# Kernel tuning notes

Hardware: AMD Instinct MI355X
Metric: run time of the kernel (lower is better)

## Reference

```python
import jax, jax.numpy as jnp
import numpy as np

N = 50000      # nodes
E = 800000     # directed edges
IN = 64        # in_dim
ED = 16        # edge_dim
H = 8          # heads
D = 32         # hdim (per-head out channels)
NM = 500       # molecules (graphs)
SLOPE = 0.2    # GATConv negative_slope
MLP_SLOPE = 0.01  # torch LeakyReLU default in the Sequential


def _glorot(k, shape, fan_in):
    return jax.random.normal(k, shape, jnp.float32) * (1.0 / np.sqrt(fan_in))


def setup_inputs() -> dict:
    key = jax.random.key(0)
    ks = jax.random.split(key, 32)
    inp = {}
    inp["x"] = jax.random.normal(ks[0], (N, IN), jnp.float32)
    inp["edge_index"] = jax.random.randint(ks[1], (2, E), 0, N)
    inp["edge_attr"] = jax.random.normal(ks[2], (E, ED), jnp.float32)
    inp["batch"] = jnp.sort(jax.random.randint(ks[3], (N,), 0, NM))
    ins = [IN, H * D, H * D]
    i = 4
    for l in range(3):
        inp[f"W{l+1}"] = _glorot(ks[i], (ins[l], H * D), ins[l]); i += 1
        inp[f"as{l+1}"] = _glorot(ks[i], (H, D), D); i += 1
        inp[f"ad{l+1}"] = _glorot(ks[i], (H, D), D); i += 1
        inp[f"We{l+1}"] = _glorot(ks[i], (ED, H * D), ED); i += 1
        inp[f"ae{l+1}"] = _glorot(ks[i], (H, D), D); i += 1
        inp[f"b{l+1}"] = jnp.zeros((H * D,), jnp.float32); i += 1
    # final MLP: 4*H*D -> 3*D -> 2*D -> 1
    inp["lw1"] = _glorot(ks[i], (4 * H * D, 3 * D), 4 * H * D); i += 1
    inp["lb1"] = jnp.zeros((3 * D,), jnp.float32)
    inp["lw2"] = _glorot(ks[i], (3 * D, 2 * D), 3 * D); i += 1
    inp["lb2"] = jnp.zeros((2 * D,), jnp.float32)
    inp["lw3"] = _glorot(ks[i], (2 * D, 1), 2 * D); i += 1
    inp["lb3"] = jnp.zeros((1,), jnp.float32)
    return inp


def _gat_conv(x, src, dst, ea, W, a_s, a_d, We, a_e, b):
    n = x.shape[0]
    xl = (x @ W).reshape(n, H, D)           # [N,H,D]
    el = (ea @ We).reshape(-1, H, D)        # [E',H,D]
    a_src = jnp.einsum('nhd,hd->nh', xl, a_s)
    a_dst = jnp.einsum('nhd,hd->nh', xl, a_d)
    a_edg = jnp.einsum('ehd,hd->eh', el, a_e)
    alpha = a_src[src] + a_dst[dst] + a_edg         # [E',H]
    alpha = jax.nn.leaky_relu(alpha, SLOPE)
    amax = jax.ops.segment_max(alpha, dst, num_segments=n)
    ex = jnp.exp(alpha - amax[dst])
    den = jax.ops.segment_sum(ex, dst, num_segments=n)
    att = ex / den[dst]                              # segment softmax over dst
    msg = xl[src] * att[:, :, None]                  # [E',H,D]
    out = jax.ops.segment_sum(msg, dst, num_segments=n)
    return out.reshape(n, H * D) + b


def reference(x, edge_index, edge_attr, batch,
              W1, as1, ad1, We1, ae1, b1,
              W2, as2, ad2, We2, ae2, b2,
              W3, as3, ad3, We3, ae3, b3,
              lw1, lb1, lw2, lb2, lw3, lb3):
    n = x.shape[0]
    src0, dst0 = edge_index[0], edge_index[1]
    loop = jnp.arange(n)
    src = jnp.concatenate([src0, loop])
    dst = jnp.concatenate([dst0, loop])
    # fill_value='add': self-loop edge_attr = sum of incoming edge_attr per node
    ea_loop = jax.ops.segment_sum(edge_attr, dst0, num_segments=n)
    ea = jnp.concatenate([edge_attr, ea_loop], axis=0)

    h1 = _gat_conv(x, src, dst, ea, W1, as1, ad1, We1, ae1, b1)
    h2 = _gat_conv(h1, src, dst, ea, W2, as2, ad2, We2, ae2, b2)
    h3 = _gat_conv(h2, src, dst, ea, W3, as3, ad3, We3, ae3, b3)

    h_pool = jax.ops.segment_sum(h3, batch, num_segments=NM)
    h_pool_ = h_pool[batch]   # == repeat_interleave(h_pool, counts) for sorted batch
    h = jnp.concatenate([h1, h2, h3, h_pool_], axis=1)
    h = jax.nn.leaky_relu(h @ lw1 + lb1, MLP_SLOPE)
    h = jax.nn.leaky_relu(h @ lw2 + lb2, MLP_SLOPE)
    h = h @ lw3 + lb3
    return jax.nn.sigmoid(h)
```

## Files before the change

kernel.cpp:

```cpp
#include <hip/hip_runtime.h>
#include <hip/hip_bf16.h>

namespace {
constexpr int kN    = 50000;
constexpr int kE    = 800000;
constexpr int kEtot = kE + kN;
constexpr int kEd   = 16;
constexpr int kH    = 8;
constexpr int kD    = 32;
constexpr int kC    = kH * kD;
constexpr int kNM   = 500;
constexpr int kNB   = (kN + 255) / 256;
constexpr int kCap  = 128;
}

typedef __attribute__((ext_vector_type(8))) _Float16 half8;
typedef __attribute__((ext_vector_type(4))) float floatx4;

__device__ __forceinline__ float h2f(ushort u) {
  union { ushort u; _Float16 h; } v;
  v.u = u;
  return (float)v.h;
}
__device__ __forceinline__ ushort f2h(float f) {
  union { _Float16 h; ushort u; } v;
  v.h = (_Float16)f;
  return v.u;
}

__global__ void gat_pre(const float* __restrict__ x,
                        const float* __restrict__ W1, const float* __restrict__ W2,
                        const float* __restrict__ W3, const float* __restrict__ lw1,
                        const float* __restrict__ lw2,
                        ushort* __restrict__ xh, ushort* __restrict__ Wt1,
                        ushort* __restrict__ Wt2, ushort* __restrict__ Wt3,
                        ushort* __restrict__ lwt1, ushort* __restrict__ lwt2p,
                        const int* __restrict__ ei, int* __restrict__ deg,
                        const float* __restrict__ We1, const float* __restrict__ ae1,
                        const float* __restrict__ We2, const float* __restrict__ ae2,
                        const float* __restrict__ We3, const float* __restrict__ ae3,
                        float* __restrict__ Q3) {
  int i = blockIdx.x * blockDim.x + threadIdx.x;
  if (i < kN * 64) { xh[i] = f2h(x[i]); return; }
  i -= kN * 64;
  if (i < 256 * 64) {
    int n = i >> 6, k = i & 63;
    Wt1[i] = f2h(W1[(long)k * 256 + n]);
    return;
  }
  i -= 256 * 64;
  if (i < 256 * 256) {
    int n = i >> 8, k = i & 255;
    Wt2[i] = f2h(W2[(long)k * 256 + n]);
    return;
  }
  i -= 256 * 256;
  if (i < 256 * 256) {
    int n = i >> 8, k = i & 255;
    Wt3[i] = f2h(W3[(long)k * 256 + n]);
    return;
  }
  i -= 256 * 256;
  if (i < 96 * 1024) {
    int n = i >> 10, k = i & 1023;
    lwt1[i] = f2h(lw1[(long)k * 96 + n]);
    return;
  }
  i -= 96 * 1024;
  if (i < 64 * 128) {
    int n = i >> 7, k = i & 127;
    lwt2p[i] = (k < 96) ? f2h(lw2[(long)k * 64 + n]) : (ushort)0;
    return;
  }
  i -= 64 * 128;
  if (i < kE) {
    atomicAdd(&deg[ei[kE + i]], 1);
    return;
  }
  i -= kE;
  if (i < 384) {
    int l = i >> 7, r = i & 127;
    const float* We = (l == 0) ? We1 : (l == 1) ? We2 : We3;
    const float* ae = (l == 0) ? ae1 : (l == 1) ? ae2 : ae3;
    int c = r >> 3, h = r & 7;
    float s = 0.f;
#pragma unroll
    for (int d = 0; d < kD; d++) s += We[c * kC + h * kD + d] * ae[h * kD + d];
    Q3[l * 128 + c * kH + h] = s;
  }
}

__global__ __launch_bounds__(256) void gat_scan_a(const int* __restrict__ deg,
                                                  int* __restrict__ offs,
                                                  int* __restrict__ bsum) {
  __shared__ int s[256];
  int b = blockIdx.x, t = threadIdx.x;
  int i = b * 256 + t;
  int v = (i < kN) ? deg[i] + 1 : 0;
  s[t] = v;
  __syncthreads();
  for (int o = 1; o < 256; o <<= 1) {
    int u = (t >= o) ? s[t - o] : 0;
    __syncthreads();
    s[t] += u;
    __syncthreads();
  }
  if (i < kN) offs[i] = s[t] - v;
  if (t == 255) bsum[b] = s[255];
}

__global__ __launch_bounds__(256) void gat_scan_b(const int* __restrict__ bsum,
                                                  int* __restrict__ bpre) {
  __shared__ int s[256];
  int t = threadIdx.x;
  int v = (t < kNB) ? bsum[t] : 0;
  s[t] = v;
  __syncthreads();
  for (int o = 1; o < 256; o <<= 1) {
    int u = (t >= o) ? s[t - o] : 0;
    __syncthreads();
    s[t] += u;
    __syncthreads();
  }
  if (t < kNB) bpre[t] = s[t] - v;
}

__global__ void gat_scan_c(int* __restrict__ offs, const int* __restrict__ bpre) {
  int i = blockIdx.x * blockDim.x + threadIdx.x;
  if (i < kN) offs[i] += bpre[blockIdx.x];
  if (i == 0) offs[kN] = kEtot;
}

__global__ void gat_fill(const int* __restrict__ ei, const int* __restrict__ offs,
                         int* __restrict__ fillc, int* __restrict__ el,
                         int* __restrict__ esrc, int* __restrict__ epos) {
  int e = blockIdx.x * blockDim.x + threadIdx.x;
  if (e >= kEtot) return;
  int s, d;
  if (e < kE) { s = ei[e]; d = ei[kE + e]; }
  else { s = d = e - kE; }
  int pos = offs[d] + atomicAdd(&fillc[d], 1);
  el[pos] = e;
  esrc[pos] = s;
  epos[e] = pos;
}

__global__ __launch_bounds__(256) void gat_aq(const int* __restrict__ el,
                                              const float* __restrict__ ea,
                                              const float* __restrict__ Q3,
                                              ushort* __restrict__ aq0,
                                              ushort* __restrict__ aq1,
                                              ushort* __restrict__ aq2) {
  __shared__ float Qs[384];
  int t = threadIdx.x;
  for (int i = t; i < 384; i += 256) Qs[i] = Q3[i];
  __syncthreads();
  int pos = blockIdx.x * blockDim.x + t;
  if (pos >= kEtot) return;
  int e = el[pos];
  long base = (long)pos * kH;
  if (e >= kE) {
    uint4 z = {0u, 0u, 0u, 0u};
    *(uint4*)(aq0 + base) = z;
    *(uint4*)(aq1 + base) = z;
    *(uint4*)(aq2 + base) = z;
    return;
  }
  float eav[kEd];
#pragma unroll
  for (int q = 0; q < kEd / 4; q++) {
    float4 v = *(const float4*)(ea + (long)e * kEd + q * 4);
    eav[q * 4 + 0] = v.x; eav[q * 4 + 1] = v.y;
    eav[q * 4 + 2] = v.z; eav[q * 4 + 3] = v.w;
  }
  ushort* outp[3] = {aq0, aq1, aq2};
#pragma unroll
  for (int l = 0; l < 3; l++) {
    union { uint4 u; ushort us[8]; } o;
#pragma unroll
    for (int h = 0; h < kH; h++) {
      float q = 0.f;
#pragma unroll
      for (int c = 0; c < kEd; c++) q += eav[c] * Qs[l * 128 + c * kH + h];
      o.us[h] = f2h(q);
    }
    *(uint4*)(outp[l] + base) = o.u;
  }
}

template <int AMODE, int COEF>
__global__ __launch_bounds__(256) void gat_gemm_mfma(
    int M, int K, int N,
    const ushort* __restrict__ A0, const ushort* __restrict__ A1,
    const ushort* __restrict__ A2, const ushort* __restrict__ A3,
    const int* __restrict__ batch,
    const ushort* __restrict__ Bt, const float* __restrict__ bias,
    float* __restrict__ C, int ldc, ushort* __restrict__ Ch, int ldch, int act,
    const float* __restrict__ as_, const float* __restrict__ ad_,
    float* __restrict__ a_src, float* __restrict__ a_dst,
    const float* __restrict__ fw3, const float* __restrict__ fb3) {
  __shared__ ushort As[8][64][8];
  __shared__ ushort Bs[8][128][8];
  int t = threadIdx.x;
  int rowBase = blockIdx.y * 64;
  int colBase = blockIdx.x * 128;
  int w = t >> 6, L = t & 63;

  floatx4 acc[8];
#pragma unroll
  for (int i = 0; i < 8; i++) acc[i] = (floatx4){0.f, 0.f, 0.f, 0.f};

  int ar = t >> 2, akq = t & 3;
  int arow = rowBase + ar;
  int bn = t >> 1, bq2 = (t & 1) * 4;
  int bok = (colBase + bn) < N;
  long brow = (long)(colBase + bn) * K;

  for (int k0 = 0; k0 < K; k0 += 64) {
#pragma unroll
    for (int half = 0; half < 2; half++) {
      int q = akq + half * 4;
      int gk = k0 + q * 8;
      uint4 av = {0u, 0u, 0u, 0u};
      if (arow < M) {
        if (AMODE == 0) {
          av = *(const uint4*)(A0 + (long)arow * K + gk);
        } else {
          int j = gk >> 8, kc = gk & 255;
          const ushort* src = (j == 0) ? A0 : (j == 1) ? A1 : (j == 2) ? A2 : A3;
          long rr = (j == 3) ? (long)batch[arow] : (long)arow;
          av = *(const uint4*)(src + rr * 256 + kc);
        }
      }
      *(uint4*)&As[q][ar][0] = av;
    }
#pragma unroll
    for (int u = 0; u < 4; u++) {
      int q = bq2 + u;
      uint4 bv = {0u, 0u, 0u, 0u};
      if (bok) bv = *(const uint4*)(Bt + brow + k0 + q * 8);
      *(uint4*)&Bs[q][bn][0] = bv;
    }
    __syncthreads();
    int mrow = w * 16 + (L & 15);
    int nl = L & 15;
#pragma unroll
    for (int half = 0; half < 2; half++) {
      int q = (L >> 4) + half * 4;
      half8 af = *(const half8*)&As[q][mrow][0];
#pragma unroll
      for (int t8 = 0; t8 < 8; t8++) {
        half8 bf = *(const half8*)&Bs[q][t8 * 16 + nl][0];
        acc[t8] = __builtin_amdgcn_mfma_f32_16x16x32_f16(af, bf, acc[t8], 0, 0, 0);
      }
    }
    __syncthreads();
  }
  int nlo = L & 15;
  int rbase = rowBase + w * 16 + (L >> 4) * 4;
  if (act == 2) {
    float dot[4] = {0.f, 0.f, 0.f, 0.f};
#pragma unroll
    for (int t8 = 0; t8 < 8; t8++) {
      int col = colBase + t8 * 16 + nlo;
      if (col >= N) continue;
      float bv = bias[col];
      float wv = fw3[col];
#pragma unroll
      for (int r = 0; r < 4; r++) {
        float v = acc[t8][r] + bv;
        v = v > 0.f ? v : 0.01f * v;
        dot[r] += v * wv;
      }
    }
#pragma unroll
    for (int msk = 1; msk < 16; msk <<= 1)
#pragma unroll
      for (int r = 0; r < 4; r++) dot[r] += __shfl_xor(dot[r], msk);
    if (nlo == 0) {
      float b3 = fb3[0];
#pragma unroll
      for (int r = 0; r < 4; r++) {
        int row = rbase + r;
        if (row < M) C[row] = 1.f / (1.f + __expf(-(dot[r] + b3)));
      }
    }
  } else {
#pragma unroll
    for (int t8 = 0; t8 < 8; t8++) {
      int col = colBase + t8 * 16 + nlo;
      if (col >= N) continue;
      float bv = bias ? bias[col] : 0.f;
#pragma unroll
      for (int r = 0; r < 4; r++) {
        int row = rbase + r;
        if (row >= M) continue;
        float v = acc[t8][r] + bv;
        if (act == 1) v = v > 0.f ? v : 0.01f * v;
        if (C) C[(long)row * ldc + col] = v;
        if (Ch) Ch[(long)row * ldch + col] = f2h(v);
      }
    }
  }
  if (COEF) {
    float ps[4][4], pd[4][4];
#pragma unroll
    for (int g = 0; g < 4; g++)
#pragma unroll
      for (int r = 0; r < 4; r++) { ps[g][r] = 0.f; pd[g][r] = 0.f; }
    int hA = colBase >> 5;
#pragma unroll
    for (int t8 = 0; t8 < 8; t8++) {
      int g = t8 >> 1;
      int widx = (t8 & 1) * 16 + nlo;
      float wsv = as_[(hA + g) * kD + widx];
      float wdv = ad_[(hA + g) * kD + widx];
#pragma unroll
      for (int r = 0; r < 4; r++) {
        ps[g][r] += acc[t8][r] * wsv;
        pd[g][r] += acc[t8][r] * wdv;
      }
    }
#pragma unroll
    for (int m = 1; m < 16; m <<= 1) {
#pragma unroll
      for (int g = 0; g < 4; g++)
#pragma unroll
        for (int r = 0; r < 4; r++) {
          ps[g][r] += __shfl_xor(ps[g][r], m);
          pd[g][r] += __shfl_xor(pd[g][r], m);
        }
    }
    if (nlo == 0) {
#pragma unroll
      for (int r = 0; r < 4; r++) {
        int row = rbase + r;
        if (row >= M) continue;
#pragma unroll
        for (int g = 0; g < 4; g++) {
          a_src[row * kH + hA + g] = ps[g][r];
          a_dst[row * kH + hA + g] = pd[g][r];
        }
      }
    }
  }
}

__global__ __launch_bounds__(256, 8) void gat_aggregate(
    const int* __restrict__ offs, const int* __restrict__ esrc,
    const int* __restrict__ epos,
    const ushort* __restrict__ aq,
    const float* __restrict__ a_src, const float* __restrict__ a_dst,
    const ushort* __restrict__ xlh, const float* __restrict__ bias,
    ushort* __restrict__ hh) {
  __shared__ float alf[4][kCap][kH];
  __shared__ int srcs[4][kCap];
  int wid = threadIdx.x >> 6;
  int n = blockIdx.x * 4 + wid;
  int L = threadIdx.x & 63;
  int lo = offs[n], hi = offs[n + 1];
  int deg = hi - lo;
  bool fits = (deg <= kCap);
  int spos = epos[kE + n];
  int hp = L & 7, sl = L >> 3;
  float adr = a_dst[n * kH + hp];
  float m = -1e30f;
  float sq = 0.f;
  if (fits) {
    for (int j = lo + sl; j < hi; j += 8) {
      int sidx = esrc[j];
      float aqv = h2f(aq[(long)j * kH + hp]);
      sq += aqv;
      float a = a_src[sidx * kH + hp] + adr + aqv;
      a = a > 0.f ? a : 0.2f * a;
      alf[wid][j - lo][hp] = a;
      if (hp == 0) srcs[wid][j - lo] = sidx;
      m = fmaxf(m, a);
    }
  } else {
    for (int j = lo + sl; j < hi; j += 8) {
      float aqv = h2f(aq[(long)j * kH + hp]);
      sq += aqv;
      float a = a_src[esrc[j] * kH + hp] + adr + aqv;
      a = a > 0.f ? a : 0.2f * a;
      m = fmaxf(m, a);
    }
  }
#pragma unroll
  for (int msk = 8; msk < 64; msk <<= 1) {
    m = fmaxf(m, __shfl_xor(m, msk));
    sq += __shfl_xor(sq, msk);
  }
  float aself = a_src[n * kH + hp] + adr + sq;
  aself = aself > 0.f ? aself : 0.2f * aself;
  m = fmaxf(m, aself);
  if (fits && sl == 0) alf[wid][spos - lo][hp] = aself;
  __syncthreads();
  float s = 0.f;
  if (fits) {
    for (int j = lo + sl; j < hi; j += 8) {
      float pp = __expf(alf[wid][j - lo][hp] - m);
      alf[wid][j - lo][hp] = pp;
      s += pp;
    }
  } else {
    for (int j = lo + sl; j < hi; j += 8) {
      float aqv = (j == spos) ? sq : h2f(aq[(long)j * kH + hp]);
      float a = a_src[esrc[j] * kH + hp] + adr + aqv;
      a = a > 0.f ? a : 0.2f * a;
      s += __expf(a - m);
    }
  }
#pragma unroll
  for (int msk = 8; msk < 64; msk <<= 1) s += __shfl_xor(s, msk);
  __syncthreads();
  int eh = L >> 5;
  int cl = L & 31;
  int c = cl * 8;
  int h = cl >> 2;
  float invs = 1.f / __shfl(s, h);
  float mh = __shfl(m, h);
  float acc[8] = {0.f, 0.f, 0.f, 0.f, 0.f, 0.f, 0.f, 0.f};
  union { uint4 u; _Float16 hf[8]; } v0, v1, v2, v3;
  if (fits) {
    int j = lo;
    for (; j + 8 <= hi; j += 8) {
      int j0 = j + eh, j1 = j + 2 + eh, j2 = j + 4 + eh, j3 = j + 6 + eh;
      int s0 = srcs[wid][j0 - lo];
      int s1 = srcs[wid][j1 - lo];
      int s2 = srcs[wid][j2 - lo];
      int s3 = srcs[wid][j3 - lo];
      float t0 = alf[wid][j0 - lo][h];
      float t1 = alf[wid][j1 - lo][h];
      float t2 = alf[wid][j2 - lo][h];
      float t3 = alf[wid][j3 - lo][h];
      v0.u = *(const uint4*)(xlh + (long)s0 * kC + c);
      v1.u = *(const uint4*)(xlh + (long)s1 * kC + c);
      v2.u = *(const uint4*)(xlh + (long)s2 * kC + c);
      v3.u = *(const uint4*)(xlh + (long)s3 * kC + c);
#pragma unroll
      for (int i = 0; i < 8; i++) acc[i] += t0 * (float)v0.hf[i];
#pragma unroll
      for (int i = 0; i < 8; i++) acc[i] += t1 * (float)v1.hf[i];
#pragma unroll
      for (int i = 0; i < 8; i++) acc[i] += t2 * (float)v2.hf[i];
#pragma unroll
      for (int i = 0; i < 8; i++) acc[i] += t3 * (float)v3.hf[i];
    }
    for (; j < hi; j += 2) {
      int jj = j + eh;
      bool valid = jj < hi;
      int idx = valid ? jj - lo : 0;
      int sn = srcs[wid][idx];
      float att = valid ? alf[wid][idx][h] : 0.f;
      v0.u = *(const uint4*)(xlh + (long)sn * kC + c);
#pragma unroll
      for (int i = 0; i < 8; i++) acc[i] += att * (float)v0.hf[i];
    }
  } else {
    float adh = a_dst[n * kH + h];
    float sqh = __shfl(sq, h);
    for (int j = lo; j < hi; j += 2) {
      int jj = j + eh;
      bool valid = jj < hi;
      int js = valid ? jj : lo;
      int sn = esrc[js];
      float aqv = (js == spos) ? sqh : h2f(aq[(long)js * kH + h]);
      float a = a_src[sn * kH + h] + adh + aqv;
      a = a > 0.f ? a : 0.2f * a;
      float att = valid ? __expf(a - mh) : 0.f;
      v0.u = *(const uint4*)(xlh + (long)sn * kC + c);
#pragma unroll
      for (int i = 0; i < 8; i++) acc[i] += att * (float)v0.hf[i];
    }
  }
#pragma unroll
  for (int i = 0; i < 8; i++) acc[i] += __shfl_xor(acc[i], 32);
  if (eh == 0) {
    float4 b0 = *(const float4*)(bias + c);
    float4 b1 = *(const float4*)(bias + c + 4);
    ushort o[8];
    o[0] = f2h(acc[0] * invs + b0.x); o[1] = f2h(acc[1] * invs + b0.y);
    o[2] = f2h(acc[2] * invs + b0.z); o[3] = f2h(acc[3] * invs + b0.w);
    o[4] = f2h(acc[4] * invs + b1.x); o[5] = f2h(acc[5] * invs + b1.y);
    o[6] = f2h(acc[6] * invs + b1.z); o[7] = f2h(acc[7] * invs + b1.w);
    *(uint4*)(hh + (long)n * kC + c) = *(uint4*)o;
  }
}

__global__ __launch_bounds__(256) void gat_pool_pad(const ushort* __restrict__ h3h,
                                                    const int* __restrict__ batch,
                                                    ushort* __restrict__ hpoolh,
                                                    ushort* __restrict__ c1h) {
  if (blockIdx.x >= kNM) {
    int i = (blockIdx.x - kNM) * 256 + threadIdx.x;
    if (i >= kN * 4) return;
    int row = i >> 2, q = i & 3;
    uint4 z = {0u, 0u, 0u, 0u};
    *(uint4*)(c1h + (long)row * 128 + 96 + q * 8) = z;
    return;
  }
  int m = blockIdx.x;
  int c = threadIdx.x;
  int lo = 0, hi = kN;
  while (lo < hi) { int mid = (lo + hi) >> 1; if (batch[mid] < m) lo = mid + 1; else hi = mid; }
  int start = lo;
  hi = kN;
  while (lo < hi) { int mid = (lo + hi) >> 1; if (batch[mid] < m + 1) lo = mid + 1; else hi = mid; }
  int end = lo;
  float s0 = 0.f, s1 = 0.f, s2 = 0.f, s3 = 0.f;
  int n = start;
  for (; n + 4 <= end; n += 4) {
    s0 += h2f(h3h[(long)n * kC + c]);
    s1 += h2f(h3h[(long)(n + 1) * kC + c]);
    s2 += h2f(h3h[(long)(n + 2) * kC + c]);
    s3 += h2f(h3h[(long)(n + 3) * kC + c]);
  }
  for (; n < end; n++) s0 += h2f(h3h[(long)n * kC + c]);
  hpoolh[(long)m * kC + c] = f2h((s0 + s1) + (s2 + s3));
}

static inline int cdiv(int a, int b) { return (a + b - 1) / b; }

extern "C" void kernel_launch(void* const* d_in, const int* in_sizes, int n_in,
                              void* d_out, int out_size, void* d_ws, size_t ws_size,
                              hipStream_t stream) {
  (void)in_sizes; (void)n_in; (void)out_size; (void)ws_size;
  const float* x = (const float*)d_in[0];
  const int* ei = (const int*)d_in[1];
  const float* ea = (const float*)d_in[2];
  const int* batch = (const int*)d_in[3];
  const float *W[3], *as_[3], *ad_[3], *We_[3], *ae_[3], *bb[3];
  for (int l = 0; l < 3; l++) {
    W[l]   = (const float*)d_in[4 + 6 * l];
    as_[l] = (const float*)d_in[5 + 6 * l];
    ad_[l] = (const float*)d_in[6 + 6 * l];
    We_[l] = (const float*)d_in[7 + 6 * l];
    ae_[l] = (const float*)d_in[8 + 6 * l];
    bb[l]  = (const float*)d_in[9 + 6 * l];
  }
  const float* lw1 = (const float*)d_in[22];
  const float* lb1 = (const float*)d_in[23];
  const float* lw2 = (const float*)d_in[24];
  const float* lb2 = (const float*)d_in[25];
  const float* lw3 = (const float*)d_in[26];
  const float* lb3 = (const float*)d_in[27];
  float* out = (float*)d_out;

  char* p = (char*)d_ws;
  auto carve = [&](size_t bytes) -> void* {
    void* r = (void*)p;
    p += (bytes + 255) & ~(size_t)255;
    return r;
  };
  ushort* aq0    = (ushort*)carve(sizeof(ushort) * (size_t)kEtot * kH);
  ushort* aq1    = (ushort*)carve(sizeof(ushort) * (size_t)kEtot * kH);
  ushort* aq2    = (ushort*)carve(sizeof(ushort) * (size_t)kEtot * kH);
  float* a_src   = (float*)carve(sizeof(float) * (size_t)kN * kH);
  float* a_dst   = (float*)carve(sizeof(float) * (size_t)kN * kH);
  float* Q3      = (float*)carve(sizeof(float) * 3 * 128);
  ushort* xh     = (ushort*)carve(sizeof(ushort) * (size_t)kN * 64);
  ushort* xlh    = (ushort*)carve(sizeof(ushort) * (size_t)kN * kC);
  ushort* h1h    = (ushort*)carve(sizeof(ushort) * (size_t)kN * kC);
  ushort* h2h    = (ushort*)carve(sizeof(ushort) * (size_t)kN * kC);
  ushort* h3h    = (ushort*)carve(sizeof(ushort) * (size_t)kN * kC);
  ushort* hpoolh = (ushort*)carve(sizeof(ushort) * (size_t)kNM * kC);
  ushort* Wt1    = (ushort*)carve(sizeof(ushort) * 64 * 256);
  ushort* Wt2    = (ushort*)carve(sizeof(ushort) * 256 * 256);
  ushort* Wt3    = (ushort*)carve(sizeof(ushort) * 256 * 256);
  ushort* lwt1   = (ushort*)carve(sizeof(ushort) * 1024 * 96);
  ushort* lwt2p  = (ushort*)carve(sizeof(ushort) * 64 * 128);
  int* deg   = (int*)carve(sizeof(int) * kN);
  int* fillc = (int*)carve(sizeof(int) * kN);
  int* offs  = (int*)carve(sizeof(int) * (kN + 1));
  int* bsum  = (int*)carve(sizeof(int) * 256);
  int* bpre  = (int*)carve(sizeof(int) * 256);
  int* el    = (int*)carve(sizeof(int) * kEtot);
  int* esrc  = (int*)carve(sizeof(int) * kEtot);
  int* epos  = (int*)carve(sizeof(int) * kEtot);
  ushort* c1h = aq0;

  hipMemsetAsync(deg, 0, sizeof(int) * kN, stream);
  hipMemsetAsync(fillc, 0, sizeof(int) * kN, stream);
  {
    int tot = kN * 64 + 256 * 64 + 2 * 256 * 256 + 96 * 1024 + 64 * 128 + kE + 384;
    gat_pre<<<cdiv(tot, 256), 256, 0, stream>>>(
        x, W[0], W[1], W[2], lw1, lw2, xh, Wt1, Wt2, Wt3, lwt1, lwt2p,
        ei, deg, We_[0], ae_[0], We_[1], ae_[1], We_[2], ae_[2], Q3);
  }

  gat_scan_a<<<kNB, 256, 0, stream>>>(deg, offs, bsum);
  gat_scan_b<<<1, 256, 0, stream>>>(bsum, bpre);
  gat_scan_c<<<kNB, 256, 0, stream>>>(offs, bpre);
  gat_fill<<<cdiv(kEtot, 256), 256, 0, stream>>>(ei, offs, fillc, el, esrc, epos);
  gat_aq<<<cdiv(kEtot, 256), 256, 0, stream>>>(el, ea, Q3, aq0, aq1, aq2);

  const ushort* hinh[3] = {xh, h1h, h2h};
  ushort* houth[3] = {h1h, h2h, h3h};
  const ushort* Wt[3] = {Wt1, Wt2, Wt3};
  const ushort* aqP[3] = {aq0, aq1, aq2};
  int kdim[3] = {64, kC, kC};
  for (int l = 0; l < 3; l++) {
    dim3 ggrid(kC / 128, cdiv(kN, 64));
    gat_gemm_mfma<0, 1><<<ggrid, 256, 0, stream>>>(
        kN, kdim[l], kC, hinh[l], nullptr, nullptr, nullptr, nullptr,
        Wt[l], nullptr, nullptr, 0, xlh, kC, 0,
        as_[l], ad_[l], a_src, a_dst, nullptr, nullptr);
    gat_aggregate<<<kN / 4, 256, 0, stream>>>(offs, esrc, epos, aqP[l], a_src, a_dst,
                                              xlh, bb[l], houth[l]);
  }

  gat_pool_pad<<<kNM + cdiv(kN * 4, 256), 256, 0, stream>>>(h3h, batch, hpoolh, c1h);

  {
    dim3 g1(1, cdiv(kN, 64));
    gat_gemm_mfma<2, 0><<<g1, 256, 0, stream>>>(
        kN, 4 * kC, 96, h1h, h2h, h3h, hpoolh, batch,
        lwt1, lb1, nullptr, 0, c1h, 128, 1,
        nullptr, nullptr, nullptr, nullptr, nullptr, nullptr);
    dim3 g2(1, cdiv(kN, 64));
    gat_gemm_mfma<0, 0><<<g2, 256, 0, stream>>>(
        kN, 128, 64, c1h, nullptr, nullptr, nullptr, nullptr,
        lwt2p, lb2, out, 1, nullptr, 0, 2,
        nullptr, nullptr, nullptr, nullptr, lw3, lb3);
  }
}
```

Baseline: 670.7 us.

## Fuse CSR fill with edge-coef pass, merge scans, fuse MLP layers into one kernel

Merges the scan's second and third stages into one kernel and folds the fillc reset into the first scan, dropping a memset and a launch. Combines edge bucketing and per-edge attention coefficient computation into a single kernel, which removes the el/epos arrays and an indirect pass over edges. Fuses the two MLP GEMMs plus the final dot and sigmoid into one kernel that keeps layer-1 activations in shared memory instead of round-tripping through global memory. Also widens the pooling kernel to 1024 threads. The fused MLP uses more shared memory per block, which may reduce occupancy.

```diff
diff --git a/kernel.cpp b/kernel.cpp
--- a/kernel.cpp
+++ b/kernel.cpp
@@ -92,11 +92,13 @@
 
 __global__ __launch_bounds__(256) void gat_scan_a(const int* __restrict__ deg,
                                                   int* __restrict__ offs,
-                                                  int* __restrict__ bsum) {
+                                                  int* __restrict__ bsum,
+                                                  int* __restrict__ fillc) {
   __shared__ int s[256];
   int b = blockIdx.x, t = threadIdx.x;
   int i = b * 256 + t;
   int v = (i < kN) ? deg[i] + 1 : 0;
+  if (i < kN) fillc[i] = 0;
   s[t] = v;
   __syncthreads();
   for (int o = 1; o < 256; o <<= 1) {
@@ -109,8 +111,8 @@
   if (t == 255) bsum[b] = s[255];
 }
 
-__global__ __launch_bounds__(256) void gat_scan_b(const int* __restrict__ bsum,
-                                                  int* __restrict__ bpre) {
+__global__ __launch_bounds__(256) void gat_scan_bc(int* __restrict__ offs,
+                                                   const int* __restrict__ bsum) {
   __shared__ int s[256];
   int t = threadIdx.x;
   int v = (t < kNB) ? bsum[t] : 0;
@@ -122,44 +124,35 @@
     s[t] += u;
     __syncthreads();
   }
-  if (t < kNB) bpre[t] = s[t] - v;
-}
-
-__global__ void gat_scan_c(int* __restrict__ offs, const int* __restrict__ bpre) {
-  int i = blockIdx.x * blockDim.x + threadIdx.x;
-  if (i < kN) offs[i] += bpre[blockIdx.x];
+  int excl = s[t] - v;
+  __syncthreads();
+  s[t] = excl;
+  __syncthreads();
+  int pre = s[blockIdx.x];
+  int i = blockIdx.x * 256 + t;
+  if (i < kN) offs[i] += pre;
   if (i == 0) offs[kN] = kEtot;
 }
 
-__global__ void gat_fill(const int* __restrict__ ei, const int* __restrict__ offs,
-                         int* __restrict__ fillc, int* __restrict__ el,
-                         int* __restrict__ esrc, int* __restrict__ epos) {
-  int e = blockIdx.x * blockDim.x + threadIdx.x;
+__global__ __launch_bounds__(256) void gat_fill_aq(
+    const int* __restrict__ ei, const int* __restrict__ offs,
+    int* __restrict__ fillc, int* __restrict__ esrc, int* __restrict__ sposA,
+    const float* __restrict__ ea, const float* __restrict__ Q3,
+    ushort* __restrict__ aq0, ushort* __restrict__ aq1, ushort* __restrict__ aq2) {
+  __shared__ float Qs[384];
+  int t = threadIdx.x;
+  for (int i = t; i < 384; i += 256) Qs[i] = Q3[i];
+  __syncthreads();
+  int e = blockIdx.x * 256 + t;
   if (e >= kEtot) return;
   int s, d;
   if (e < kE) { s = ei[e]; d = ei[kE + e]; }
   else { s = d = e - kE; }
   int pos = offs[d] + atomicAdd(&fillc[d], 1);
-  el[pos] = e;
   esrc[pos] = s;
-  epos[e] = pos;
-}
-
-__global__ __launch_bounds__(256) void gat_aq(const int* __restrict__ el,
-                                              const float* __restrict__ ea,
-                                              const float* __restrict__ Q3,
-                                              ushort* __restrict__ aq0,
-                                              ushort* __restrict__ aq1,
-                                              ushort* __restrict__ aq2) {
-  __shared__ float Qs[384];
-  int t = threadIdx.x;
-  for (int i = t; i < 384; i += 256) Qs[i] = Q3[i];
-  __syncthreads();
-  int pos = blockIdx.x * blockDim.x + t;
-  if (pos >= kEtot) return;
-  int e = el[pos];
   long base = (long)pos * kH;
   if (e >= kE) {
+    sposA[e - kE] = pos;
     uint4 z = {0u, 0u, 0u, 0u};
     *(uint4*)(aq0 + base) = z;
     *(uint4*)(aq1 + base) = z;
@@ -188,17 +181,13 @@
   }
 }
 
-template <int AMODE, int COEF>
 __global__ __launch_bounds__(256) void gat_gemm_mfma(
-    int M, int K, int N,
-    const ushort* __restrict__ A0, const ushort* __restrict__ A1,
-    const ushort* __restrict__ A2, const ushort* __restrict__ A3,
-    const int* __restrict__ batch,
-    const ushort* __restrict__ Bt, const float* __restrict__ bias,
-    float* __restrict__ C, int ldc, ushort* __restrict__ Ch, int ldch, int act,
+    int M, int K,
+    const ushort* __restrict__ A0,
+    const ushort* __restrict__ Bt,
+    ushort* __restrict__ Ch, int ldch,
     const float* __restrict__ as_, const float* __restrict__ ad_,
-    float* __restrict__ a_src, float* __restrict__ a_dst,
-    const float* __restrict__ fw3, const float* __restrict__ fb3) {
+    float* __restrict__ a_src, float* __restrict__ a_dst) {
   __shared__ ushort As[8][64][8];
   __shared__ ushort Bs[8][128][8];
   int t = threadIdx.x;
@@ -213,7 +202,6 @@
   int ar = t >> 2, akq = t & 3;
   int arow = rowBase + ar;
   int bn = t >> 1, bq2 = (t & 1) * 4;
-  int bok = (colBase + bn) < N;
   long brow = (long)(colBase + bn) * K;
 
   for (int k0 = 0; k0 < K; k0 += 64) {
@@ -222,23 +210,13 @@
       int q = akq + half * 4;
       int gk = k0 + q * 8;
       uint4 av = {0u, 0u, 0u, 0u};
-      if (arow < M) {
-        if (AMODE == 0) {
-          av = *(const uint4*)(A0 + (long)arow * K + gk);
-        } else {
-          int j = gk >> 8, kc = gk & 255;
-          const ushort* src = (j == 0) ? A0 : (j == 1) ? A1 : (j == 2) ? A2 : A3;
-          long rr = (j == 3) ? (long)batch[arow] : (long)arow;
-          av = *(const uint4*)(src + rr * 256 + kc);
-        }
-      }
+      if (arow < M) av = *(const uint4*)(A0 + (long)arow * K + gk);
       *(uint4*)&As[q][ar][0] = av;
     }
 #pragma unroll
     for (int u = 0; u < 4; u++) {
       int q = bq2 + u;
-      uint4 bv = {0u, 0u, 0u, 0u};
-      if (bok) bv = *(const uint4*)(Bt + brow + k0 + q * 8);
+      uint4 bv = *(const uint4*)(Bt + brow + k0 + q * 8);
       *(uint4*)&Bs[q][bn][0] = bv;
     }
     __syncthreads();
@@ -258,51 +236,17 @@
   }
   int nlo = L & 15;
   int rbase = rowBase + w * 16 + (L >> 4) * 4;
-  if (act == 2) {
-    float dot[4] = {0.f, 0.f, 0.f, 0.f};
-#pragma unroll
-    for (int t8 = 0; t8 < 8; t8++) {
-      int col = colBase + t8 * 16 + nlo;
-      if (col >= N) continue;
-      float bv = bias[col];
-      float wv = fw3[col];
-#pragma unroll
-      for (int r = 0; r < 4; r++) {
-        float v = acc[t8][r] + bv;
-        v = v > 0.f ? v : 0.01f * v;
-        dot[r] += v * wv;
-      }
-    }
-#pragma unroll
-    for (int msk = 1; msk < 16; msk <<= 1)
-#pragma unroll
-      for (int r = 0; r < 4; r++) dot[r] += __shfl_xor(dot[r], msk);
-    if (nlo == 0) {
-      float b3 = fb3[0];
-#pragma unroll
-      for (int r = 0; r < 4; r++) {
-        int row = rbase + r;
-        if (row < M) C[row] = 1.f / (1.f + __expf(-(dot[r] + b3)));
-      }
-    }
-  } else {
-#pragma unroll
-    for (int t8 = 0; t8 < 8; t8++) {
-      int col = colBase + t8 * 16 + nlo;
-      if (col >= N) continue;
-      float bv = bias ? bias[col] : 0.f;
-#pragma unroll
-      for (int r = 0; r < 4; r++) {
-        int row = rbase + r;
-        if (row >= M) continue;
-        float v = acc[t8][r] + bv;
-        if (act == 1) v = v > 0.f ? v : 0.01f * v;
-        if (C) C[(long)row * ldc + col] = v;
-        if (Ch) Ch[(long)row * ldch + col] = f2h(v);
-      }
-    }
-  }
-  if (COEF) {
+#pragma unroll
+  for (int t8 = 0; t8 < 8; t8++) {
+    int col = colBase + t8 * 16 + nlo;
+#pragma unroll
+    for (int r = 0; r < 4; r++) {
+      int row = rbase + r;
+      if (row >= M) continue;
+      Ch[(long)row * ldch + col] = f2h(acc[t8][r]);
+    }
+  }
+  {
     float ps[4][4], pd[4][4];
 #pragma unroll
     for (int g = 0; g < 4; g++)
@@ -348,7 +292,7 @@
 
 __global__ __launch_bounds__(256, 8) void gat_aggregate(
     const int* __restrict__ offs, const int* __restrict__ esrc,
-    const int* __restrict__ epos,
+    const int* __restrict__ sposA,
     const ushort* __restrict__ aq,
     const float* __restrict__ a_src, const float* __restrict__ a_dst,
     const ushort* __restrict__ xlh, const float* __restrict__ bias,
@@ -361,7 +305,7 @@
   int lo = offs[n], hi = offs[n + 1];
   int deg = hi - lo;
   bool fits = (deg <= kCap);
-  int spos = epos[kE + n];
+  int spos = sposA[n];
   int hp = L & 7, sl = L >> 3;
   float adr = a_dst[n * kH + hp];
   float m = -1e30f;
@@ -488,20 +432,13 @@
   }
 }
 
-__global__ __launch_bounds__(256) void gat_pool_pad(const ushort* __restrict__ h3h,
-                                                    const int* __restrict__ batch,
-                                                    ushort* __restrict__ hpoolh,
-                                                    ushort* __restrict__ c1h) {
-  if (blockIdx.x >= kNM) {
-    int i = (blockIdx.x - kNM) * 256 + threadIdx.x;
-    if (i >= kN * 4) return;
-    int row = i >> 2, q = i & 3;
-    uint4 z = {0u, 0u, 0u, 0u};
-    *(uint4*)(c1h + (long)row * 128 + 96 + q * 8) = z;
-    return;
-  }
+__global__ __launch_bounds__(1024) void gat_pool(const ushort* __restrict__ h3h,
+                                                 const int* __restrict__ batch,
+                                                 ushort* __restrict__ hpoolh) {
+  __shared__ float red[3][256];
   int m = blockIdx.x;
-  int c = threadIdx.x;
+  int c = threadIdx.x & 255;
+  int g = threadIdx.x >> 8;
   int lo = 0, hi = kN;
   while (lo < hi) { int mid = (lo + hi) >> 1; if (batch[mid] < m) lo = mid + 1; else hi = mid; }
   int start = lo;
@@ -509,15 +446,150 @@
   while (lo < hi) { int mid = (lo + hi) >> 1; if (batch[mid] < m + 1) lo = mid + 1; else hi = mid; }
   int end = lo;
   float s0 = 0.f, s1 = 0.f, s2 = 0.f, s3 = 0.f;
-  int n = start;
-  for (; n + 4 <= end; n += 4) {
+  int n = start + g;
+  for (; n + 12 < end; n += 16) {
     s0 += h2f(h3h[(long)n * kC + c]);
-    s1 += h2f(h3h[(long)(n + 1) * kC + c]);
-    s2 += h2f(h3h[(long)(n + 2) * kC + c]);
-    s3 += h2f(h3h[(long)(n + 3) * kC + c]);
-  }
-  for (; n < end; n++) s0 += h2f(h3h[(long)n * kC + c]);
-  hpoolh[(long)m * kC + c] = f2h((s0 + s1) + (s2 + s3));
+    s1 += h2f(h3h[(long)(n + 4) * kC + c]);
+    s2 += h2f(h3h[(long)(n + 8) * kC + c]);
+    s3 += h2f(h3h[(long)(n + 12) * kC + c]);
+  }
+  for (; n < end; n += 4) s0 += h2f(h3h[(long)n * kC + c]);
+  float s = (s0 + s1) + (s2 + s3);
+  if (g > 0) red[g - 1][c] = s;
+  __syncthreads();
+  if (g == 0)
+    hpoolh[(long)m * kC + c] = f2h(s + red[0][c] + red[1][c] + red[2][c]);
+}
+
+__global__ __launch_bounds__(256) void gat_mlp(
+    const ushort* __restrict__ h1h, const ushort* __restrict__ h2h,
+    const ushort* __restrict__ h3h, const ushort* __restrict__ hpoolh,
+    const int* __restrict__ batch,
+    const ushort* __restrict__ lwt1, const float* __restrict__ lb1,
+    const ushort* __restrict__ lwt2p, const float* __restrict__ lb2,
+    const float* __restrict__ lw3, const float* __restrict__ lb3,
+    float* __restrict__ out) {
+  __shared__ ushort As[8][64][8];
+  __shared__ ushort Bs[8][128][8];
+  __shared__ ushort C1s[16][64][8];
+  __shared__ ushort B2s[16][64][8];
+  constexpr int K = 1024;
+  int t = threadIdx.x;
+  int rowBase = blockIdx.x * 64;
+  int w = t >> 6, L = t & 63;
+
+  floatx4 acc[8];
+#pragma unroll
+  for (int i = 0; i < 8; i++) acc[i] = (floatx4){0.f, 0.f, 0.f, 0.f};
+
+  int ar = t >> 2, akq = t & 3;
+  int arow = rowBase + ar;
+  int bn = t >> 1, bq2 = (t & 1) * 4;
+  bool bok = bn < 96;
+  long brow = (long)bn * K;
+
+  for (int k0 = 0; k0 < K; k0 += 64) {
+#pragma unroll
+    for (int half = 0; half < 2; half++) {
+      int q = akq + half * 4;
+      int gk = k0 + q * 8;
+      uint4 av = {0u, 0u, 0u, 0u};
+      if (arow < kN) {
+        int j = gk >> 8, kc = gk & 255;
+        const ushort* src = (j == 0) ? h1h : (j == 1) ? h2h : (j == 2) ? h3h : hpoolh;
+        long rr = (j == 3) ? (long)batch[arow] : (long)arow;
+        av = *(const uint4*)(src + rr * 256 + kc);
+      }
+      *(uint4*)&As[q][ar][0] = av;
+    }
+#pragma unroll
+    for (int u = 0; u < 4; u++) {
+      int q = bq2 + u;
+      uint4 bv = {0u, 0u, 0u, 0u};
+      if (bok) bv = *(const uint4*)(lwt1 + brow + k0 + q * 8);
+      *(uint4*)&Bs[q][bn][0] = bv;
+    }
+    __syncthreads();
+    int mrow = w * 16 + (L & 15);
+    int nl = L & 15;
+#pragma unroll
+    for (int half = 0; half < 2; half++) {
+      int q = (L >> 4) + half * 4;
+      half8 af = *(const half8*)&As[q][mrow][0];
+#pragma unroll
+      for (int t8 = 0; t8 < 8; t8++) {
+        half8 bf = *(const half8*)&Bs[q][t8 * 16 + nl][0];
+        acc[t8] = __builtin_amdgcn_mfma_f32_16x16x32_f16(af, bf, acc[t8], 0, 0, 0);
+      }
+    }
+    __syncthreads();
+  }
+  int nlo = L & 15;
+  int lrbase = w * 16 + (L >> 4) * 4;
+#pragma unroll
+  for (int t8 = 0; t8 < 8; t8++) {
+    int col = t8 * 16 + nlo;
+    float bv = (col < 96) ? lb1[col] : 0.f;
+#pragma unroll
+    for (int r = 0; r < 4; r++) {
+      float v = acc[t8][r] + bv;
+      v = v > 0.f ? v : 0.01f * v;
+      C1s[col >> 3][lrbase + r][col & 7] = f2h(v);
+    }
+  }
+  {
+    int n2 = t >> 2, u0 = (t & 3) * 4;
+#pragma unroll
+    for (int u = 0; u < 4; u++) {
+      int q = u0 + u;
+      *(uint4*)&B2s[q][n2][0] = *(const uint4*)(lwt2p + (long)n2 * 128 + q * 8);
+    }
+  }
+  __syncthreads();
+  floatx4 acc2[4];
+#pragma unroll
+  for (int i = 0; i < 4; i++) acc2[i] = (floatx4){0.f, 0.f, 0.f, 0.f};
+  {
+    int mrow = w * 16 + (L & 15);
+    int nl = L & 15;
+#pragma unroll
+    for (int ks = 0; ks < 4; ks++) {
+      int q = (L >> 4) + ks * 4;
+      half8 af = *(const half8*)&C1s[q][mrow][0];
+#pragma unroll
+      for (int nf = 0; nf < 4; nf++) {
+        half8 bf = *(const half8*)&B2s[q][nf * 16 + nl][0];
+        acc2[nf] = __builtin_amdgcn_mfma_f32_16x16x32_f16(af, bf, acc2[nf], 0, 0, 0);
+      }
+    }
+  }
+  {
+    float dot[4] = {0.f, 0.f, 0.f, 0.f};
+#pragma unroll
+    for (int nf = 0; nf < 4; nf++) {
+      int col = nf * 16 + nlo;
+      float bv = lb2[col];
+      float wv = lw3[col];
+#pragma unroll
+      for (int r = 0; r < 4; r++) {
+        float v = acc2[nf][r] + bv;
+        v = v > 0.f ? v : 0.01f * v;
+        dot[r] += v * wv;
+      }
+    }
+#pragma unroll
+    for (int msk = 1; msk < 16; msk <<= 1)
+#pragma unroll
+      for (int r = 0; r < 4; r++) dot[r] += __shfl_xor(dot[r], msk);
+    if (nlo == 0) {
+      float b3 = lb3[0];
+#pragma unroll
+      for (int r = 0; r < 4; r++) {
+        int row = rowBase + lrbase + r;
+        if (row < kN) out[row] = 1.f / (1.f + __expf(-(dot[r] + b3)));
+      }
+    }
+  }
 }
 
 static inline int cdiv(int a, int b) { return (a + b - 1) / b; }
@@ -574,14 +646,10 @@
   int* fillc = (int*)carve(sizeof(int) * kN);
   int* offs  = (int*)carve(sizeof(int) * (kN + 1));
   int* bsum  = (int*)carve(sizeof(int) * 256);
-  int* bpre  = (int*)carve(sizeof(int) * 256);
-  int* el    = (int*)carve(sizeof(int) * kEtot);
   int* esrc  = (int*)carve(sizeof(int) * kEtot);
-  int* epos  = (int*)carve(sizeof(int) * kEtot);
-  ushort* c1h = aq0;
+  int* sposA = (int*)carve(sizeof(int) * kN);
 
   hipMemsetAsync(deg, 0, sizeof(int) * kN, stream);
-  hipMemsetAsync(fillc, 0, sizeof(int) * kN, stream);
   {
     int tot = kN * 64 + 256 * 64 + 2 * 256 * 256 + 96 * 1024 + 64 * 128 + kE + 384;
     gat_pre<<<cdiv(tot, 256), 256, 0, stream>>>(
@@ -589,11 +657,10 @@
         ei, deg, We_[0], ae_[0], We_[1], ae_[1], We_[2], ae_[2], Q3);
   }
 
-  gat_scan_a<<<kNB, 256, 0, stream>>>(deg, offs, bsum);
-  gat_scan_b<<<1, 256, 0, stream>>>(bsum, bpre);
-  gat_scan_c<<<kNB, 256, 0, stream>>>(offs, bpre);
-  gat_fill<<<cdiv(kEtot, 256), 256, 0, stream>>>(ei, offs, fillc, el, esrc, epos);
-  gat_aq<<<cdiv(kEtot, 256), 256, 0, stream>>>(el, ea, Q3, aq0, aq1, aq2);
+  gat_scan_a<<<kNB, 256, 0, stream>>>(deg, offs, bsum, fillc);
+  gat_scan_bc<<<kNB, 256, 0, stream>>>(offs, bsum);
+  gat_fill_aq<<<cdiv(kEtot, 256), 256, 0, stream>>>(ei, offs, fillc, esrc, sposA,
+                                                    ea, Q3, aq0, aq1, aq2);
 
   const ushort* hinh[3] = {xh, h1h, h2h};
   ushort* houth[3] = {h1h, h2h, h3h};
@@ -602,26 +669,16 @@
   int kdim[3] = {64, kC, kC};
   for (int l = 0; l < 3; l++) {
     dim3 ggrid(kC / 128, cdiv(kN, 64));
-    gat_gemm_mfma<0, 1><<<ggrid, 256, 0, stream>>>(
-        kN, kdim[l], kC, hinh[l], nullptr, nullptr, nullptr, nullptr,
-        Wt[l], nullptr, nullptr, 0, xlh, kC, 0,
-        as_[l], ad_[l], a_src, a_dst, nullptr, nullptr);
-    gat_aggregate<<<kN / 4, 256, 0, stream>>>(offs, esrc, epos, aqP[l], a_src, a_dst,
+    gat_gemm_mfma<<<ggrid, 256, 0, stream>>>(
+        kN, kdim[l], hinh[l], Wt[l], xlh, kC,
+        as_[l], ad_[l], a_src, a_dst);
+    gat_aggregate<<<kN / 4, 256, 0, stream>>>(offs, esrc, sposA, aqP[l], a_src, a_dst,
                                               xlh, bb[l], houth[l]);
   }
 
-  gat_pool_pad<<<kNM + cdiv(kN * 4, 256), 256, 0, stream>>>(h3h, batch, hpoolh, c1h);
-
-  {
-    dim3 g1(1, cdiv(kN, 64));
-    gat_gemm_mfma<2, 0><<<g1, 256, 0, stream>>>(
-        kN, 4 * kC, 96, h1h, h2h, h3h, hpoolh, batch,
-        lwt1, lb1, nullptr, 0, c1h, 128, 1,
-        nullptr, nullptr, nullptr, nullptr, nullptr, nullptr);
-    dim3 g2(1, cdiv(kN, 64));
-    gat_gemm_mfma<0, 0><<<g2, 256, 0, stream>>>(
-        kN, 128, 64, c1h, nullptr, nullptr, nullptr, nullptr,
-        lwt2p, lb2, out, 1, nullptr, 0, 2,
-        nullptr, nullptr, nullptr, nullptr, lw3, lb3);
-  }
-}
+  gat_pool<<<kNM, 1024, 0, stream>>>(h3h, batch, hpoolh);
+
+  gat_mlp<<<cdiv(kN, 64), 256, 0, stream>>>(
+      h1h, h2h, h3h, hpoolh, batch,
+      lwt1, lb1, lwt2p, lb2, lw3, lb3, out);
+}
```

After: 617.2 us. -8.0%, faster.
